# Performance work log

Measured on AMD Instinct MI355X. Metric: run time of the kernel, lower is better.

The kernel has to match this reference:

```python
import jax, jax.numpy as jnp
import numpy as np

OBS_DIM = 256
HIDDEN = 512

def setup_inputs() -> dict:
    key = jax.random.key(0)
    ks = jax.random.split(key, 7)
    s_x = 1.0 / np.sqrt(OBS_DIM)
    s_h = 1.0 / np.sqrt(HIDDEN)
    return {
        "x": jax.random.normal(ks[0], (32, 2048, OBS_DIM), dtype=jnp.float32),
        "Whx_w": jax.random.uniform(ks[1], (HIDDEN, OBS_DIM), jnp.float32, -s_x, s_x),
        "Whx_b": jax.random.uniform(ks[2], (HIDDEN,), jnp.float32, -s_x, s_x),
        "Whh_w": jax.random.uniform(ks[3], (HIDDEN, HIDDEN), jnp.float32, -s_h, s_h),
        "Whh_b": jax.random.uniform(ks[4], (HIDDEN,), jnp.float32, -s_h, s_h),
        "Woh_w": jax.random.uniform(ks[5], (HIDDEN, HIDDEN), jnp.float32, -s_h, s_h),
        "Woh_b": jax.random.uniform(ks[6], (HIDDEN,), jnp.float32, -s_h, s_h),
    }

def reference(x, Whx_w, Whx_b, Whh_w, Whh_b, Woh_w, Woh_b):
    # x: (B, L, D). Precompute input projection for all timesteps (one big GEMM).
    B, L, D = x.shape
    xp = jnp.einsum("bld,hd->blh", x, Whx_w) + Whx_b  # (B, L, H)

    def step(h_prev, xp_t):
        h_t = jax.nn.relu(xp_t + h_prev @ Whh_w.T + Whh_b)
        y_t = jax.nn.softmax(h_t @ Woh_w.T + Woh_b, axis=1)
        return h_t, (y_t, h_t)

    h0 = jnp.zeros((B, HIDDEN), dtype=x.dtype)
    _, (ys, hs) = jax.lax.scan(step, h0, jnp.swapaxes(xp, 0, 1))  # scan over L
    output_arr = jnp.swapaxes(ys, 0, 1)  # (B, L, H)
    hidden_arr = jnp.swapaxes(hs, 0, 1)  # (B, L, H)
    return output_arr, hidden_arr
```

## Files before the change

kernel.cpp:

```cpp
#include <hip/hip_runtime.h>

#define H    512
#define DOBS 256
#define BATCH 32
#define SEQ  2048
#define NSLICE 8
#define NS 64

typedef float f8 __attribute__((ext_vector_type(8)));

__global__ __launch_bounds__(256) void transpose_k(const float* __restrict__ W,
                                                   float* __restrict__ Wt) {
  __shared__ float tile[32][33];
  int tx  = threadIdx.x & 31;
  int ty4 = (threadIdx.x >> 5) * 4;
  int bx = blockIdx.x * 32;
  int by = blockIdx.y * 32;
#pragma unroll
  for (int i = 0; i < 4; ++i)
    tile[ty4 + i][tx] = W[(by + ty4 + i) * H + bx + tx];
  __syncthreads();
#pragma unroll
  for (int i = 0; i < 4; ++i)
    Wt[(bx + ty4 + i) * H + by + tx] = tile[tx][ty4 + i];
}

__global__ __launch_bounds__(256) void gemm_bias_k(const float* __restrict__ A,
                                                   const float* __restrict__ B,
                                                   const float* __restrict__ bias,
                                                   float* __restrict__ C,
                                                   int M, int N, int K) {
  __shared__ float As[16][132];
  __shared__ float Bs[16][132];
  const int m0 = blockIdx.x * 128;
  const int n0 = blockIdx.y * 128;
  const int t  = threadIdx.x;
  const int tm = (t >> 4) * 4;
  const int tn = (t & 15) * 4;
  const int lrow = t >> 2;
  const int lcol = (t & 3) * 4;

  float acc[8][8] = {};

  for (int k0 = 0; k0 < K; k0 += 16) {
    float4 a0 = *(const float4*)&A[(size_t)(m0 + lrow)      * K + k0 + lcol];
    float4 a1 = *(const float4*)&A[(size_t)(m0 + lrow + 64) * K + k0 + lcol];
    float4 b0 = *(const float4*)&B[(size_t)(n0 + lrow)      * K + k0 + lcol];
    float4 b1 = *(const float4*)&B[(size_t)(n0 + lrow + 64) * K + k0 + lcol];
    __syncthreads();
    As[lcol + 0][lrow] = a0.x; As[lcol + 1][lrow] = a0.y;
    As[lcol + 2][lrow] = a0.z; As[lcol + 3][lrow] = a0.w;
    As[lcol + 0][lrow + 64] = a1.x; As[lcol + 1][lrow + 64] = a1.y;
    As[lcol + 2][lrow + 64] = a1.z; As[lcol + 3][lrow + 64] = a1.w;
    Bs[lcol + 0][lrow] = b0.x; Bs[lcol + 1][lrow] = b0.y;
    Bs[lcol + 2][lrow] = b0.z; Bs[lcol + 3][lrow] = b0.w;
    Bs[lcol + 0][lrow + 64] = b1.x; Bs[lcol + 1][lrow + 64] = b1.y;
    Bs[lcol + 2][lrow + 64] = b1.z; Bs[lcol + 3][lrow + 64] = b1.w;
    __syncthreads();
#pragma unroll
    for (int k = 0; k < 16; ++k) {
      float4 aA = *(const float4*)&As[k][tm];
      float4 aB = *(const float4*)&As[k][tm + 64];
      float4 bA = *(const float4*)&Bs[k][tn];
      float4 bB = *(const float4*)&Bs[k][tn + 64];
      float av[8] = {aA.x, aA.y, aA.z, aA.w, aB.x, aB.y, aB.z, aB.w};
      float bv[8] = {bA.x, bA.y, bA.z, bA.w, bB.x, bB.y, bB.z, bB.w};
#pragma unroll
      for (int i = 0; i < 8; ++i)
#pragma unroll
        for (int j = 0; j < 8; ++j)
          acc[i][j] = fmaf(av[i], bv[j], acc[i][j]);
    }
  }

  float4 bbA = *(const float4*)&bias[n0 + tn];
  float4 bbB = *(const float4*)&bias[n0 + tn + 64];
#pragma unroll
  for (int i = 0; i < 8; ++i) {
    int row = m0 + ((i < 4) ? (tm + i) : (64 + tm + i - 4));
    float4 c0, c1;
    c0.x = acc[i][0] + bbA.x; c0.y = acc[i][1] + bbA.y;
    c0.z = acc[i][2] + bbA.z; c0.w = acc[i][3] + bbA.w;
    c1.x = acc[i][4] + bbB.x; c1.y = acc[i][5] + bbB.y;
    c1.z = acc[i][6] + bbB.z; c1.w = acc[i][7] + bbB.w;
    *(float4*)&C[(size_t)row * N + n0 + tn]      = c0;
    *(float4*)&C[(size_t)row * N + n0 + tn + 64] = c1;
  }
}

__global__ __launch_bounds__(256, 1) void rnn_rec_k(float* __restrict__ hid,
                                                    float* __restrict__ exch,
                                                    const float* __restrict__ Wt,
                                                    const float* __restrict__ bias) {
  const int b     = blockIdx.x & (BATCH - 1);
  const int slice = blockIdx.x >> 5;
  const int n0    = slice * NS;
  const int tid   = threadIdx.x;
  const int w     = tid >> 6;
  const int l     = tid & 63;

  __shared__ __align__(16) float shh[H];
  __shared__ float sh_part[2][4][NS];

  float* hb = hid  + (size_t)b * SEQ * H;
  float* eb = exch + (size_t)b * SEQ * H;

  f8 Wv[16];
  {
    const float* wp = Wt + (size_t)(w * 128) * H + n0 + l;
#pragma unroll
    for (int i = 0; i < 16; ++i) {
#pragma unroll
      for (int j = 0; j < 8; ++j)
        Wv[i][j] = wp[(size_t)(i * 8 + j) * H];
    }
  }
  const float bn = bias[n0 + l];

  const float4* sh4 = (const float4*)&shh[w * 128];

  float xp_cur = 0.f, xp_nxt = 0.f;
  if (w == 0) xp_cur = hb[n0 + l];
  float kp0 = 0.f, kp1 = 0.f;

  for (int t = 0; t < SEQ; ++t) {
    float v0 = 0.f, v1 = 0.f;
    if (t > 0) {
      const float* ep = eb + (size_t)(t - 1) * H + w * 128;
      for (;;) {
        v0 = __hip_atomic_load(ep + l,      __ATOMIC_RELAXED, __HIP_MEMORY_SCOPE_AGENT);
        v1 = __hip_atomic_load(ep + 64 + l, __ATOMIC_RELAXED, __HIP_MEMORY_SCOPE_AGENT);
        if (!__any(!(v0 >= 1.0f && v1 >= 1.0f))) break;
      }
      asm volatile("" :: "v"(kp0), "v"(kp1) : "memory");
      shh[w * 128 + l]      = v0 - 1.0f;
      shh[w * 128 + 64 + l] = v1 - 1.0f;
      asm volatile("s_waitcnt lgkmcnt(0)" ::: "memory");
    } else {
      asm volatile("" ::: "memory");
    }

    if (t + 1 < SEQ) {
      const float* pf = eb + (size_t)t * H + w * 128;
      kp0 = pf[l];
      kp1 = pf[64 + l];
      if (w == 0) xp_nxt = hb[(size_t)(t + 1) * H + n0 + l];
    }

    float partial = 0.f;
    if (t > 0) {
      float a0 = 0.f, a1 = 0.f, a2 = 0.f, a3 = 0.f;
#pragma unroll
      for (int i = 0; i < 16; ++i) {
        float4 hA = sh4[2 * i];
        float4 hB = sh4[2 * i + 1];
        a0 = fmaf(Wv[i][0], hA.x, a0);
        a1 = fmaf(Wv[i][1], hA.y, a1);
        a2 = fmaf(Wv[i][2], hA.z, a2);
        a3 = fmaf(Wv[i][3], hA.w, a3);
        a0 = fmaf(Wv[i][4], hB.x, a0);
        a1 = fmaf(Wv[i][5], hB.y, a1);
        a2 = fmaf(Wv[i][6], hB.z, a2);
        a3 = fmaf(Wv[i][7], hB.w, a3);
      }
      partial = (a0 + a1) + (a2 + a3);
    }

    sh_part[t & 1][w][l] = partial;
    asm volatile("s_waitcnt lgkmcnt(0)" ::: "memory");
    __builtin_amdgcn_s_barrier();
    asm volatile("" ::: "memory");

    if (w == 0) {
      float v = sh_part[t & 1][0][l] + sh_part[t & 1][1][l]
              + sh_part[t & 1][2][l] + sh_part[t & 1][3][l] + xp_cur + bn;
      float hv = fmaxf(v, 0.f);
      __hip_atomic_store(&eb[(size_t)t * H + n0 + l], hv + 1.0f,
                         __ATOMIC_RELAXED, __HIP_MEMORY_SCOPE_AGENT);
      hb[(size_t)t * H + n0 + l] = hv;
    }
    xp_cur = xp_nxt;
  }
}

__global__ __launch_bounds__(256) void softmax_k(float* __restrict__ Z) {
  __shared__ float smax[4];
  __shared__ float ssum[4];
  float* row = Z + (size_t)blockIdx.x * H;
  const int t = threadIdx.x;
  float2 v = *(float2*)&row[2 * t];
  float m = fmaxf(v.x, v.y);
#pragma unroll
  for (int o = 32; o > 0; o >>= 1) m = fmaxf(m, __shfl_xor(m, o, 64));
  const int wave = t >> 6, lane = t & 63;
  if (lane == 0) smax[wave] = m;
  __syncthreads();
  m = fmaxf(fmaxf(smax[0], smax[1]), fmaxf(smax[2], smax[3]));
  const float LOG2E = 1.44269504088896f;
  float ex = exp2f((v.x - m) * LOG2E);
  float ey = exp2f((v.y - m) * LOG2E);
  float s = ex + ey;
#pragma unroll
  for (int o = 32; o > 0; o >>= 1) s += __shfl_xor(s, o, 64);
  if (lane == 0) ssum[wave] = s;
  __syncthreads();
  float inv = 1.0f / (ssum[0] + ssum[1] + ssum[2] + ssum[3]);
  float2 r;
  r.x = ex * inv;
  r.y = ey * inv;
  *(float2*)&row[2 * t] = r;
}

extern "C" void kernel_launch(void* const* d_in, const int* in_sizes, int n_in,
                              void* d_out, int out_size, void* d_ws, size_t ws_size,
                              hipStream_t stream) {
  const float* x     = (const float*)d_in[0];
  const float* Whx_w = (const float*)d_in[1];
  const float* Whx_b = (const float*)d_in[2];
  const float* Whh_w = (const float*)d_in[3];
  const float* Whh_b = (const float*)d_in[4];
  const float* Woh_w = (const float*)d_in[5];
  const float* Woh_b = (const float*)d_in[6];

  float* y   = (float*)d_out;
  float* hid = (float*)d_out + (size_t)BATCH * SEQ * H;
  float* Wt  = (float*)d_ws;

  const int M = BATCH * SEQ;

  transpose_k<<<dim3(16, 16), 256, 0, stream>>>(Whh_w, Wt);
  gemm_bias_k<<<dim3(M / 128, H / 128), 256, 0, stream>>>(x, Whx_w, Whx_b, hid, M, H, DOBS);
  rnn_rec_k<<<BATCH * NSLICE, 256, 0, stream>>>(hid, y, Wt, Whh_b);
  gemm_bias_k<<<dim3(M / 128, H / 128), 256, 0, stream>>>(hid, Woh_w, Woh_b, y, M, H, H);
  softmax_k<<<M, 256, 0, stream>>>(y);
}
```

Baseline: 3.577 ms.

## Fuse output projection into recurrent kernel and drop separate transpose and GEMM

The recurrent kernel now loads both Whh and Woh rows directly into registers, with four lanes splitting each output neuron's dot product and combining via shuffles. This removes the shared-memory partial-sum reduction barrier and lets each lane group write h_t directly. The output logits are computed in the idle time after publishing h_t and written lazily into the exchange buffer two steps later, with the final step kept in a workspace. This eliminates the transpose kernel and the second full GEMM, at the cost of doubling register weight storage and adding work to the latency-critical loop.

```diff
diff --git a/kernel.cpp b/kernel.cpp
--- a/kernel.cpp
+++ b/kernel.cpp
@@ -9,21 +9,8 @@
 
 typedef float f8 __attribute__((ext_vector_type(8)));
 
-__global__ __launch_bounds__(256) void transpose_k(const float* __restrict__ W,
-                                                   float* __restrict__ Wt) {
-  __shared__ float tile[32][33];
-  int tx  = threadIdx.x & 31;
-  int ty4 = (threadIdx.x >> 5) * 4;
-  int bx = blockIdx.x * 32;
-  int by = blockIdx.y * 32;
-#pragma unroll
-  for (int i = 0; i < 4; ++i)
-    tile[ty4 + i][tx] = W[(by + ty4 + i) * H + bx + tx];
-  __syncthreads();
-#pragma unroll
-  for (int i = 0; i < 4; ++i)
-    Wt[(bx + ty4 + i) * H + by + tx] = tile[tx][ty4 + i];
-}
+#define PLD(p)    __hip_atomic_load((p), __ATOMIC_RELAXED, __HIP_MEMORY_SCOPE_AGENT)
+#define PST(p, v) __hip_atomic_store((p), (v), __ATOMIC_RELAXED, __HIP_MEMORY_SCOPE_AGENT)
 
 __global__ __launch_bounds__(256) void gemm_bias_k(const float* __restrict__ A,
                                                    const float* __restrict__ B,
@@ -90,105 +77,166 @@
 
 __global__ __launch_bounds__(256, 1) void rnn_rec_k(float* __restrict__ hid,
                                                     float* __restrict__ exch,
-                                                    const float* __restrict__ Wt,
-                                                    const float* __restrict__ bias) {
+                                                    const float* __restrict__ Whh,
+                                                    const float* __restrict__ bh,
+                                                    const float* __restrict__ Woh,
+                                                    const float* __restrict__ bo,
+                                                    float* __restrict__ zlast) {
   const int b     = blockIdx.x & (BATCH - 1);
   const int slice = blockIdx.x >> 5;
   const int n0    = slice * NS;
   const int tid   = threadIdx.x;
   const int w     = tid >> 6;
   const int l     = tid & 63;
-
-  __shared__ __align__(16) float shh[H];
-  __shared__ float sh_part[2][4][NS];
+  const int c     = l & 3;
+  const int g     = l >> 2;
+  const int n     = n0 + w * 16 + g;
+  const bool lead = (c == 0);
+
+  __shared__ __align__(16) float shh[2][4 * 132];
 
   float* hb = hid  + (size_t)b * SEQ * H;
   float* eb = exch + (size_t)b * SEQ * H;
 
-  f8 Wv[16];
+  f8 Wh[16], Wo[16];
   {
-    const float* wp = Wt + (size_t)(w * 128) * H + n0 + l;
+    const float* ph = Whh + (size_t)n * H + c * 128;
+    const float* po = Woh + (size_t)n * H + c * 128;
 #pragma unroll
     for (int i = 0; i < 16; ++i) {
-#pragma unroll
-      for (int j = 0; j < 8; ++j)
-        Wv[i][j] = wp[(size_t)(i * 8 + j) * H];
-    }
-  }
-  const float bn = bias[n0 + l];
-
-  const float4* sh4 = (const float4*)&shh[w * 128];
-
-  float xp_cur = 0.f, xp_nxt = 0.f;
-  if (w == 0) xp_cur = hb[n0 + l];
-  float kp0 = 0.f, kp1 = 0.f;
+      Wh[i] = *(const f8*)(ph + 8 * i);
+      Wo[i] = *(const f8*)(po + 8 * i);
+    }
+  }
+  const float bnh = bh[n];
+  const float bno = bo[n];
+
+  float xp_cur = hb[n];
+  float xp_nxt = 0.f;
+  float v0 = 0.f, v1 = 0.f;
+  float zheld = 0.f;
 
   for (int t = 0; t < SEQ; ++t) {
-    float v0 = 0.f, v1 = 0.f;
+    float* buf = shh[t & 1];
     if (t > 0) {
       const float* ep = eb + (size_t)(t - 1) * H + w * 128;
-      for (;;) {
-        v0 = __hip_atomic_load(ep + l,      __ATOMIC_RELAXED, __HIP_MEMORY_SCOPE_AGENT);
-        v1 = __hip_atomic_load(ep + 64 + l, __ATOMIC_RELAXED, __HIP_MEMORY_SCOPE_AGENT);
-        if (!__any(!(v0 >= 1.0f && v1 >= 1.0f))) break;
+      while (__any(!(v0 >= 1.0f && v1 >= 1.0f))) {
+        v0 = PLD(ep + l);
+        v1 = PLD(ep + 64 + l);
       }
-      asm volatile("" :: "v"(kp0), "v"(kp1) : "memory");
-      shh[w * 128 + l]      = v0 - 1.0f;
-      shh[w * 128 + 64 + l] = v1 - 1.0f;
+      buf[w * 132 + l]      = v0 - 1.0f;
+      buf[w * 132 + 64 + l] = v1 - 1.0f;
       asm volatile("s_waitcnt lgkmcnt(0)" ::: "memory");
-    } else {
+      __builtin_amdgcn_s_barrier();
       asm volatile("" ::: "memory");
-    }
-
-    if (t + 1 < SEQ) {
-      const float* pf = eb + (size_t)t * H + w * 128;
-      kp0 = pf[l];
-      kp1 = pf[64 + l];
-      if (w == 0) xp_nxt = hb[(size_t)(t + 1) * H + n0 + l];
-    }
-
-    float partial = 0.f;
+      if (t >= 2 && lead) eb[(size_t)(t - 2) * H + n] = zheld;
+    }
+
+    float r = 0.f;
     if (t > 0) {
+      const float4* hp = (const float4*)(buf + c * 132);
       float a0 = 0.f, a1 = 0.f, a2 = 0.f, a3 = 0.f;
 #pragma unroll
       for (int i = 0; i < 16; ++i) {
-        float4 hA = sh4[2 * i];
-        float4 hB = sh4[2 * i + 1];
-        a0 = fmaf(Wv[i][0], hA.x, a0);
-        a1 = fmaf(Wv[i][1], hA.y, a1);
-        a2 = fmaf(Wv[i][2], hA.z, a2);
-        a3 = fmaf(Wv[i][3], hA.w, a3);
-        a0 = fmaf(Wv[i][4], hB.x, a0);
-        a1 = fmaf(Wv[i][5], hB.y, a1);
-        a2 = fmaf(Wv[i][6], hB.z, a2);
-        a3 = fmaf(Wv[i][7], hB.w, a3);
+        float4 hA = hp[2 * i];
+        float4 hB = hp[2 * i + 1];
+        a0 = fmaf(Wh[i][0], hA.x, a0);
+        a1 = fmaf(Wh[i][1], hA.y, a1);
+        a2 = fmaf(Wh[i][2], hA.z, a2);
+        a3 = fmaf(Wh[i][3], hA.w, a3);
+        a0 = fmaf(Wh[i][4], hB.x, a0);
+        a1 = fmaf(Wh[i][5], hB.y, a1);
+        a2 = fmaf(Wh[i][6], hB.z, a2);
+        a3 = fmaf(Wh[i][7], hB.w, a3);
       }
-      partial = (a0 + a1) + (a2 + a3);
-    }
-
-    sh_part[t & 1][w][l] = partial;
+      r = (a0 + a1) + (a2 + a3);
+      r += __shfl_xor(r, 1, 64);
+      r += __shfl_xor(r, 2, 64);
+    }
+    if (lead) {
+      float hv = fmaxf(r + xp_cur + bnh, 0.f);
+      PST(&eb[(size_t)t * H + n], hv + 1.0f);
+      hb[(size_t)t * H + n] = hv;
+    }
+
+    {
+      const float* ep = eb + (size_t)t * H + w * 128;
+      v0 = PLD(ep + l);
+      v1 = PLD(ep + 64 + l);
+      if (t + 1 < SEQ) xp_nxt = hb[(size_t)(t + 1) * H + n];
+    }
+
+    if (t > 0) {
+      const float4* hp = (const float4*)(buf + c * 132);
+      float a0 = 0.f, a1 = 0.f, a2 = 0.f, a3 = 0.f;
+#pragma unroll
+      for (int i = 0; i < 16; ++i) {
+        float4 hA = hp[2 * i];
+        float4 hB = hp[2 * i + 1];
+        a0 = fmaf(Wo[i][0], hA.x, a0);
+        a1 = fmaf(Wo[i][1], hA.y, a1);
+        a2 = fmaf(Wo[i][2], hA.z, a2);
+        a3 = fmaf(Wo[i][3], hA.w, a3);
+        a0 = fmaf(Wo[i][4], hB.x, a0);
+        a1 = fmaf(Wo[i][5], hB.y, a1);
+        a2 = fmaf(Wo[i][6], hB.z, a2);
+        a3 = fmaf(Wo[i][7], hB.w, a3);
+      }
+      float zr = (a0 + a1) + (a2 + a3);
+      zr += __shfl_xor(zr, 1, 64);
+      zr += __shfl_xor(zr, 2, 64);
+      zheld = zr + bno;
+    }
+    xp_cur = xp_nxt;
+  }
+
+  {
+    float* buf = shh[SEQ & 1];
+    const float* ep = eb + (size_t)(SEQ - 1) * H + w * 128;
+    while (__any(!(v0 >= 1.0f && v1 >= 1.0f))) {
+      v0 = PLD(ep + l);
+      v1 = PLD(ep + 64 + l);
+    }
+    buf[w * 132 + l]      = v0 - 1.0f;
+    buf[w * 132 + 64 + l] = v1 - 1.0f;
     asm volatile("s_waitcnt lgkmcnt(0)" ::: "memory");
     __builtin_amdgcn_s_barrier();
     asm volatile("" ::: "memory");
-
-    if (w == 0) {
-      float v = sh_part[t & 1][0][l] + sh_part[t & 1][1][l]
-              + sh_part[t & 1][2][l] + sh_part[t & 1][3][l] + xp_cur + bn;
-      float hv = fmaxf(v, 0.f);
-      __hip_atomic_store(&eb[(size_t)t * H + n0 + l], hv + 1.0f,
-                         __ATOMIC_RELAXED, __HIP_MEMORY_SCOPE_AGENT);
-      hb[(size_t)t * H + n0 + l] = hv;
-    }
-    xp_cur = xp_nxt;
-  }
-}
-
-__global__ __launch_bounds__(256) void softmax_k(float* __restrict__ Z) {
+    if (lead) eb[(size_t)(SEQ - 2) * H + n] = zheld;
+
+    const float4* hp = (const float4*)(buf + c * 132);
+    float a0 = 0.f, a1 = 0.f, a2 = 0.f, a3 = 0.f;
+#pragma unroll
+    for (int i = 0; i < 16; ++i) {
+      float4 hA = hp[2 * i];
+      float4 hB = hp[2 * i + 1];
+      a0 = fmaf(Wo[i][0], hA.x, a0);
+      a1 = fmaf(Wo[i][1], hA.y, a1);
+      a2 = fmaf(Wo[i][2], hA.z, a2);
+      a3 = fmaf(Wo[i][3], hA.w, a3);
+      a0 = fmaf(Wo[i][4], hB.x, a0);
+      a1 = fmaf(Wo[i][5], hB.y, a1);
+      a2 = fmaf(Wo[i][6], hB.z, a2);
+      a3 = fmaf(Wo[i][7], hB.w, a3);
+    }
+    float zr = (a0 + a1) + (a2 + a3);
+    zr += __shfl_xor(zr, 1, 64);
+    zr += __shfl_xor(zr, 2, 64);
+    if (lead) zlast[(size_t)b * H + n] = zr + bno;
+  }
+}
+
+__global__ __launch_bounds__(256) void softmax_k(float* __restrict__ Z,
+                                                 const float* __restrict__ zlast) {
   __shared__ float smax[4];
   __shared__ float ssum[4];
-  float* row = Z + (size_t)blockIdx.x * H;
+  const int r  = blockIdx.x;
+  const int bb = r >> 11;
+  const int tt = r & (SEQ - 1);
+  float* row = Z + (size_t)r * H;
+  const float* src = (tt == SEQ - 1) ? (zlast + (size_t)bb * H) : row;
   const int t = threadIdx.x;
-  float2 v = *(float2*)&row[2 * t];
+  float2 v = *(const float2*)&src[2 * t];
   float m = fmaxf(v.x, v.y);
 #pragma unroll
   for (int o = 32; o > 0; o >>= 1) m = fmaxf(m, __shfl_xor(m, o, 64));
@@ -205,10 +253,10 @@
   if (lane == 0) ssum[wave] = s;
   __syncthreads();
   float inv = 1.0f / (ssum[0] + ssum[1] + ssum[2] + ssum[3]);
-  float2 r;
-  r.x = ex * inv;
-  r.y = ey * inv;
-  *(float2*)&row[2 * t] = r;
+  float2 out;
+  out.x = ex * inv;
+  out.y = ey * inv;
+  *(float2*)&row[2 * t] = out;
 }
 
 extern "C" void kernel_launch(void* const* d_in, const int* in_sizes, int n_in,
@@ -222,15 +270,13 @@
   const float* Woh_w = (const float*)d_in[5];
   const float* Woh_b = (const float*)d_in[6];
 
-  float* y   = (float*)d_out;
-  float* hid = (float*)d_out + (size_t)BATCH * SEQ * H;
-  float* Wt  = (float*)d_ws;
+  float* y     = (float*)d_out;
+  float* hid   = (float*)d_out + (size_t)BATCH * SEQ * H;
+  float* zlast = (float*)d_ws;
 
   const int M = BATCH * SEQ;
 
-  transpose_k<<<dim3(16, 16), 256, 0, stream>>>(Whh_w, Wt);
   gemm_bias_k<<<dim3(M / 128, H / 128), 256, 0, stream>>>(x, Whx_w, Whx_b, hid, M, H, DOBS);
-  rnn_rec_k<<<BATCH * NSLICE, 256, 0, stream>>>(hid, y, Wt, Whh_b);
-  gemm_bias_k<<<dim3(M / 128, H / 128), 256, 0, stream>>>(hid, Woh_w, Woh_b, y, M, H, H);
-  softmax_k<<<M, 256, 0, stream>>>(y);
-}
+  rnn_rec_k<<<BATCH * NSLICE, 256, 0, stream>>>(hid, y, Whh_w, Whh_b, Woh_w, Woh_b, zlast);
+  softmax_k<<<M, 256, 0, stream>>>(y, zlast);
+}
```

Result: slower. 5.734 ms (+60.3%).
